# Performance work log

Hardware: AMD Instinct MI355X
Metric: run time of the kernel (lower is better)

Reference implementation:

```python
import jax, jax.numpy as jnp
import numpy as np

B, S, H = 2, 1024, 1024
NH, HD = 8, 128
E, TOPK, MI = 8, 2, 1024
SI = 2 * MI  # shared experts intermediate (n_shared_experts=2)
EPS = 1e-6
THETA = 10000.0


def setup_inputs() -> dict:
    key = jax.random.key(0)
    ks = jax.random.split(key, 16)
    w = lambda k, shp: (0.02 * jax.random.normal(k, shp, dtype=jnp.float32))
    # RoPE tables [S, HD]
    inv_freq = 1.0 / (THETA ** (np.arange(0, HD, 2, dtype=np.float32) / HD))
    t = np.arange(S, dtype=np.float32)
    freqs = np.outer(t, inv_freq)
    emb = np.concatenate([freqs, freqs], axis=-1)
    return {
        "hidden_states": jax.random.normal(ks[0], (B, S, H), dtype=jnp.float32),
        "ln1_w": jnp.ones((H,), jnp.float32),
        "ln2_w": jnp.ones((H,), jnp.float32),
        "q_w": w(ks[1], (H, H)),
        "k_w": w(ks[2], (H, H)),
        "v_w": w(ks[3], (H, H)),
        "o_w": w(ks[4], (H, H)),
        "cos": jnp.asarray(np.cos(emb), jnp.float32),
        "sin": jnp.asarray(np.sin(emb), jnp.float32),
        "gate_w": w(ks[5], (E, H)),
        "eg_w": w(ks[6], (E, MI, H)),
        "eu_w": w(ks[7], (E, MI, H)),
        "ed_w": w(ks[8], (E, H, MI)),
        "sg_w": w(ks[9], (SI, H)),
        "su_w": w(ks[10], (SI, H)),
        "sd_w": w(ks[11], (H, SI)),
    }


def _rmsnorm(x, w):
    return x * jax.lax.rsqrt(jnp.mean(x * x, axis=-1, keepdims=True) + EPS) * w


def _rotate_half(x):
    x1, x2 = jnp.split(x, 2, axis=-1)
    return jnp.concatenate([-x2, x1], axis=-1)


def _attention(x, q_w, k_w, v_w, o_w, cos, sin):
    b, s, h = x.shape
    q = (x @ q_w.T).reshape(b, s, NH, HD)
    k = (x @ k_w.T).reshape(b, s, NH, HD)
    v = (x @ v_w.T).reshape(b, s, NH, HD)
    c = cos[None, :s, None, :]
    sn = sin[None, :s, None, :]
    q = q * c + _rotate_half(q) * sn
    k = k * c + _rotate_half(k) * sn
    scores = jnp.einsum("bqhd,bkhd->bhqk", q, k) / jnp.sqrt(jnp.float32(HD))
    causal = jnp.tril(jnp.ones((s, s), dtype=bool))
    scores = jnp.where(causal[None, None], scores, -jnp.inf)
    p = jax.nn.softmax(scores, axis=-1)
    out = jnp.einsum("bhqk,bkhd->bqhd", p, v).reshape(b, s, h)
    return out @ o_w.T


def _mlp(x, gw, uw, dw):
    return (jax.nn.silu(x @ gw.T) * (x @ uw.T)) @ dw.T


def _moe(x, gate_w, eg_w, eu_w, ed_w, sg_w, su_w, sd_w):
    b, s, h = x.shape
    xt = x.reshape(-1, h)                              # [T, H]
    T = xt.shape[0]
    probs = jax.nn.softmax(xt @ gate_w.T, axis=-1)     # [T, E]
    rw, idx = jax.lax.top_k(probs, TOPK)               # [T, K]
    rw = rw / (jnp.sum(rw, axis=-1, keepdims=True) + 1e-20)  # norm_topk_prob
    # dense combine weights [T, E] (zero for unselected experts)
    w_full = jnp.zeros((T, E), xt.dtype).at[jnp.arange(T)[:, None], idx].add(rw)
    # dense all-expert compute, masked-combined (faithful to per-token loop math)
    g = jax.nn.silu(jnp.einsum("th,eih->tei", xt, eg_w))
    u = jnp.einsum("th,eih->tei", xt, eu_w)
    y = jnp.einsum("tei,ehi->teh", g * u, ed_w)        # [T, E, H]
    routed = jnp.einsum("teh,te->th", y, w_full)
    shared = _mlp(xt, sg_w, su_w, sd_w)
    return (routed + shared).reshape(b, s, h)


def reference(hidden_states, ln1_w, ln2_w, q_w, k_w, v_w, o_w, cos, sin,
              gate_w, eg_w, eu_w, ed_w, sg_w, su_w, sd_w):
    x = hidden_states
    x = x + _attention(_rmsnorm(x, ln1_w), q_w, k_w, v_w, o_w, cos, sin)
    x = x + _moe(_rmsnorm(x, ln2_w), gate_w, eg_w, eu_w, ed_w, sg_w, su_w, sd_w)
    return x
```

## Files before the change

### kernel.cpp

```cpp
#include <hip/hip_runtime.h>

#define B_   2
#define S_   1024
#define H_   1024
#define NH_  8
#define HD_  128
#define E_   8
#define MI_  1024
#define SI_  2048
#define T_   2048
#define CAP_ 2048

typedef unsigned short u16;
typedef __attribute__((ext_vector_type(4))) float f32x4;
typedef __attribute__((ext_vector_type(4))) unsigned short u16x4;
typedef __attribute__((ext_vector_type(8))) unsigned short u16x8;
typedef __attribute__((ext_vector_type(8))) __bf16 bf16x8;

__device__ __forceinline__ u16 f2bf(float f) {
  unsigned int u = __builtin_bit_cast(unsigned int, f);
  u = (u + 0x7fffu + ((u >> 16) & 1u)) >> 16;
  return (u16)u;
}
__device__ __forceinline__ float bf2f(u16 u) {
  return __builtin_bit_cast(float, (unsigned int)u << 16);
}
__device__ __forceinline__ float wave_sum(float v) {
#pragma unroll
  for (int o = 32; o; o >>= 1) v += __shfl_down(v, o, 64);
  return v;
}
__device__ __forceinline__ void gll16(const u16* g, u16* l) {
  __builtin_amdgcn_global_load_lds((const __attribute__((address_space(1))) void*)g,
                                   (__attribute__((address_space(3))) void*)l, 16, 0, 0);
}

__device__ __forceinline__ void cvt_moe_rows(
    int row0, int tid,
    const float* __restrict__ eg_w, const float* __restrict__ eu_w,
    const float* __restrict__ ed_w, const float* __restrict__ sg_w,
    const float* __restrict__ su_w, const float* __restrict__ sd_w,
    u16* __restrict__ egu, u16* __restrict__ edb,
    u16* __restrict__ sgu, u16* __restrict__ sdb) {
  const float* src[8];
  u16* dst[8];
#pragma unroll
  for (int g = 0; g < 8; g++) {
    int row = row0 + g;
    if (row < 20480) {
      int rel = row - 4096;
      int zu = rel >= 8192;
      int r = rel & 8191;
      int e = r >> 10, i = r & 1023;
      int orow = (i >> 4) * 32 + (i & 15) + (zu ? 16 : 0);
      src[g] = (zu ? eu_w : eg_w) + (long)r * 1024;
      dst[g] = egu + ((long)e * 2048 + orow) * 1024;
    } else if (row < 28672) {
      long f = (long)(row - 20480) * 1024;
      src[g] = ed_w + f;
      dst[g] = edb + f;
    } else if (row < 32768) {
      int rel = row - 28672;
      int zu = rel >= 2048;
      int i = rel & 2047;
      int orow = (i >> 4) * 32 + (i & 15) + (zu ? 16 : 0);
      src[g] = (zu ? su_w : sg_w) + (long)i * 1024;
      dst[g] = sgu + (long)orow * 1024;
    } else {
      long f = (long)(row - 32768) * 1024;
      src[g] = sd_w + f;
      dst[g] = sdb + f;
    }
  }
  f32x4 v[8];
#pragma unroll
  for (int g = 0; g < 8; g++)
    v[g] = __builtin_nontemporal_load((const f32x4*)src[g] + tid);
#pragma unroll
  for (int g = 0; g < 8; g++) {
    u16x4 o;
#pragma unroll
    for (int c = 0; c < 4; c++) o[c] = f2bf(v[g][c]);
    ((u16x4*)dst[g])[tid] = o;
  }
}

__global__ void cvt_all(const float* __restrict__ q_w, const float* __restrict__ k_w,
                        const float* __restrict__ v_w, const float* __restrict__ o_w,
                        u16* __restrict__ qwb,
                        const float* __restrict__ hidden, const float* __restrict__ ln1w,
                        u16* __restrict__ xn) {
  int bid = blockIdx.x, tid = threadIdx.x;
  if (bid >= 512) {
    int t = bid - 512;
    f32x4 v = ((const f32x4*)(hidden + (long)t * H_))[tid];
    float ss = v[0]*v[0] + v[1]*v[1] + v[2]*v[2] + v[3]*v[3];
    __shared__ float red[4];
    float s = wave_sum(ss);
    if ((tid & 63) == 0) red[tid >> 6] = s;
    __syncthreads();
    float r = rsqrtf((red[0] + red[1] + red[2] + red[3]) * (1.0f / H_) + 1e-6f);
    f32x4 wv = ((const f32x4*)ln1w)[tid];
    u16x4 o;
#pragma unroll
    for (int c = 0; c < 4; c++) o[c] = f2bf(v[c] * r * wv[c]);
    ((u16x4*)(xn + (long)t * H_))[tid] = o;
    return;
  }
  const float* src[8];
  u16* dst[8];
#pragma unroll
  for (int g = 0; g < 8; g++) {
    int row = bid * 8 + g;
    int seg = row >> 10;
    const float* in = (seg == 0) ? q_w : (seg == 1) ? k_w : (seg == 2) ? v_w : o_w;
    src[g] = in + (long)(row & 1023) * 1024;
    dst[g] = qwb + (long)row * 1024;
  }
  f32x4 v[8];
#pragma unroll
  for (int g = 0; g < 8; g++)
    v[g] = __builtin_nontemporal_load((const f32x4*)src[g] + tid);
#pragma unroll
  for (int g = 0; g < 8; g++) {
    u16x4 o;
#pragma unroll
    for (int c = 0; c < 4; c++) o[c] = f2bf(v[g][c]);
    ((u16x4*)dst[g])[tid] = o;
  }
}

__global__ void rmsnorm2_gate(const float* __restrict__ x1, const float* __restrict__ ln2w,
                              const float* __restrict__ gw, u16* __restrict__ xn,
                              int* __restrict__ eidx, float* __restrict__ aw) {
  int t = blockIdx.x, tid = threadIdx.x;
  int lane = tid & 63, wave = tid >> 6;
  f32x4 v = ((const f32x4*)(x1 + (long)t * H_))[tid];
  float ss = v[0]*v[0] + v[1]*v[1] + v[2]*v[2] + v[3]*v[3];
  __shared__ float redS[4];
  __shared__ float redE[4][E_];
  float s = wave_sum(ss);
  if (lane == 0) redS[wave] = s;
  __syncthreads();
  float r = rsqrtf((redS[0] + redS[1] + redS[2] + redS[3]) * (1.0f / H_) + 1e-6f);
  f32x4 wv = ((const f32x4*)ln2w)[tid];
  float xv[4];
  u16x4 o;
#pragma unroll
  for (int c = 0; c < 4; c++) { xv[c] = v[c] * r * wv[c]; o[c] = f2bf(xv[c]); }
  ((u16x4*)(xn + (long)t * H_))[tid] = o;
  float acc[E_];
#pragma unroll
  for (int e = 0; e < E_; e++) {
    f32x4 g = ((const f32x4*)(gw + (long)e * H_))[tid];
    acc[e] = xv[0]*g[0] + xv[1]*g[1] + xv[2]*g[2] + xv[3]*g[3];
  }
#pragma unroll
  for (int e = 0; e < E_; e++) acc[e] = wave_sum(acc[e]);
  if (lane == 0)
#pragma unroll
    for (int e = 0; e < E_; e++) redE[wave][e] = acc[e];
  __syncthreads();
  if (tid == 0) {
    float l[E_];
#pragma unroll
    for (int e = 0; e < E_; e++) l[e] = redE[0][e] + redE[1][e] + redE[2][e] + redE[3][e];
    float mx = l[0];
#pragma unroll
    for (int e = 1; e < E_; e++) mx = fmaxf(mx, l[e]);
    float p[E_], z = 0.f;
#pragma unroll
    for (int e = 0; e < E_; e++) { p[e] = __expf(l[e] - mx); z += p[e]; }
    int e0 = 0;
#pragma unroll
    for (int e = 1; e < E_; e++) if (p[e] > p[e0]) e0 = e;
    int e1 = (e0 == 0) ? 1 : 0;
#pragma unroll
    for (int e = 0; e < E_; e++) if (e != e0 && p[e] > p[e1]) e1 = e;
    float q0 = p[e0] / z, q1 = p[e1] / z;
    float invs = 1.0f / (q0 + q1 + 1e-20f);
    eidx[t * 2] = e0;
    eidx[t * 2 + 1] = e1;
    aw[t * 2] = q0 * invs;
    aw[t * 2 + 1] = q1 * invs;
  }
}

__global__ __launch_bounds__(256) void route_scan(const int* __restrict__ eidx,
                                                  int* __restrict__ arow,
                                                  int* __restrict__ cursor,
                                                  int* __restrict__ itok,
                                                  int* __restrict__ wlist,
                                                  int* __restrict__ wl256) {
  __shared__ int sc[E_][256];
  int tid = threadIdx.x;
  unsigned c0 = 0, c1 = 0;
  int ebuf[16];
#pragma unroll
  for (int i = 0; i < 16; i++) {
    int e = eidx[tid * 16 + i];
    ebuf[i] = e;
    if (e < 4) c0 += 1u << (8 * e); else c1 += 1u << (8 * (e - 4));
  }
#pragma unroll
  for (int e = 0; e < E_; e++)
    sc[e][tid] = (e < 4) ? (int)((c0 >> (8 * e)) & 0xff) : (int)((c1 >> (8 * (e - 4))) & 0xff);
  __syncthreads();
  for (int st = 1; st < 256; st <<= 1) {
    int v[E_];
#pragma unroll
    for (int e = 0; e < E_; e++) v[e] = (tid >= st) ? sc[e][tid - st] : 0;
    __syncthreads();
#pragma unroll
    for (int e = 0; e < E_; e++) sc[e][tid] += v[e];
    __syncthreads();
  }
  if (tid == 255) {
    int w = 0, w2 = 0;
#pragma unroll
    for (int e = 0; e < E_; e++) {
      int cnt = sc[e][255];
      cursor[e] = cnt;
      int cc = min(cnt, CAP_);
      int nt = (cc + 127) >> 7;
      for (int mt = 0; mt < nt; mt++) wlist[w++] = (e << 8) | mt;
      int nt2 = (cc + 255) >> 8;
      for (int mt = 0; mt < nt2; mt++) wl256[w2++] = (e << 8) | mt;
    }
    for (int mt = 0; mt < 16; mt++) wlist[w++] = (1 << 16) | mt;
    for (; w < 56; w++) wlist[w] = -1;
    for (int mt = 0; mt < 8; mt++) wl256[w2++] = (1 << 16) | mt;
    for (; w2 < 32; w2++) wl256[w2] = -1;
  }
  int base[E_];
#pragma unroll
  for (int e = 0; e < E_; e++) {
    int own = (e < 4) ? (int)((c0 >> (8 * e)) & 0xff) : (int)((c1 >> (8 * (e - 4))) & 0xff);
    base[e] = sc[e][tid] - own;
  }
  __syncthreads();
#pragma unroll
  for (int e = 0; e < E_; e++) sc[e][tid] = base[e];
  __syncthreads();
  unsigned r0 = 0, r1 = 0;
#pragma unroll
  for (int i = 0; i < 16; i++) {
    int e = ebuf[i];
    int run = (e < 4) ? (int)((r0 >> (8 * e)) & 0xff) : (int)((r1 >> (8 * (e - 4))) & 0xff);
    int row = e * CAP_ + sc[e][tid] + run;
    arow[tid * 16 + i] = row;
    itok[row] = (tid * 16 + i) >> 1;
    if (e < 4) r0 += 1u << (8 * e); else r1 += 1u << (8 * (e - 4));
  }
}

__global__ void rope_vtrans(const u16* __restrict__ qkvb, const float* __restrict__ cs,
                            const float* __restrict__ sn, u16* __restrict__ qb,
                            u16* __restrict__ kb, u16* __restrict__ vt) {
  int bid = blockIdx.x, tid = threadIdx.x;
  if (bid < 1024) {
    int z = bid >> 9;
    const u16* src = qkvb + (long)z * 2097152;
    u16* dstb = z ? kb : qb;
    int rb = (bid & 511) * 32 + (tid >> 3);
    int u = tid & 7;
    int h = rb & 7, bs = rb >> 3, s = bs & 1023, b = bs >> 10;
    const u16* row = src + (long)rb * 128;
    int d0 = u * 8;
    u16x8 v1 = *(const u16x8*)(row + d0);
    u16x8 v2 = *(const u16x8*)(row + d0 + 64);
    const float* c1 = cs + s * 128 + d0;
    const float* s1 = sn + s * 128 + d0;
    u16x8 o1, o2;
#pragma unroll
    for (int c = 0; c < 8; c++) {
      float a = bf2f(v1[c]), q2 = bf2f(v2[c]);
      o1[c] = f2bf(a * c1[c] - q2 * s1[c]);
      o2[c] = f2bf(q2 * c1[c + 64] + a * s1[c + 64]);
    }
    u16* orow = dstb + ((long)((b * NH_ + h) * S_ + s)) * HD_;
    *(u16x8*)(orow + d0) = o1;
    *(u16x8*)(orow + d0 + 64) = o2;
  } else {
    int vb = bid - 1024;
    int bh = vb >> 5;
    int rem = vb & 31;
    int s0 = (rem >> 1) * 64, d0 = (rem & 1) * 64;
    int b = bh >> 3, h = bh & 7;
    __shared__ u16 tile[64][68];
    const u16* vsrc = qkvb + 2 * 2097152;
#pragma unroll
    for (int it = 0; it < 4; it++) {
      int idx = it * 256 + tid;
      int r = idx >> 4, c = (idx & 15) * 4;
      u16x4 vv = *(const u16x4*)(vsrc + (((long)(b * S_ + s0 + r)) * NH_ + h) * HD_ + d0 + c);
      *(u16x4*)&tile[r][c] = vv;
    }
    __syncthreads();
#pragma unroll
    for (int it = 0; it < 4; it++) {
      int idx = it * 256 + tid;
      int dr = idx >> 4, sc = (idx & 15) * 4;
      u16x4 ov;
#pragma unroll
      for (int k = 0; k < 4; k++) ov[k] = tile[sc + k][dr];
      *(u16x4*)(vt + ((long)bh * HD_ + d0 + dr) * S_ + s0 + sc) = ov;
    }
  }
}

__global__ __launch_bounds__(256) void flash_cvt(
    const u16* __restrict__ qb, const u16* __restrict__ kb,
    const u16* __restrict__ vt, u16* __restrict__ Po,
    float* __restrict__ Pm, float* __restrict__ Pl,
    const float* __restrict__ eg_w, const float* __restrict__ eu_w,
    const float* __restrict__ ed_w, const float* __restrict__ sg_w,
    const float* __restrict__ su_w, const float* __restrict__ sd_w,
    u16* __restrict__ egu, u16* __restrict__ edb,
    u16* __restrict__ sgu, u16* __restrict__ sdb) {
  int bid = blockIdx.x;
  int tid = threadIdx.x;
  if (bid >= 640) {
    int row0 = 4096 + (bid - 640) * 8;
    cvt_moe_rows(row0, tid, eg_w, eu_w, ed_w, sg_w, su_w, sd_w, egu, edb, sgu, sdb);
    return;
  }
  int item = bid % 40;
  int bh = bid / 40;
  int qt, ch;
  if (item < 4)       { qt = item;                    ch = 0; }
  else if (item < 12) { qt = 4 + ((item - 4) >> 1);   ch = (item - 4) & 1; }
  else if (item < 24) { qt = 8 + (item - 12) / 3;     ch = (item - 12) % 3; }
  else                { qt = 12 + ((item - 24) >> 2); ch = (item - 24) & 3; }
  int j0 = ch * 4, j1 = min(j0 + 4, qt + 1);

  int wavei = tid >> 6, lane = tid & 63;
  int la = lane & 15, qd = lane >> 4;

  __shared__ __align__(16) u16 Ks[64 * 128];
  __shared__ __align__(16) u16 Vs[128 * 64];
  __shared__ __align__(16) u16 Ps[4][16 * 64];

  bf16x8 qf[4];
  const u16* qrow = qb + ((long)bh * S_ + qt * 64 + wavei * 16 + la) * HD_;
#pragma unroll
  for (int ks = 0; ks < 4; ks++)
    qf[ks] = *(const bf16x8*)(qrow + ks * 32 + qd * 8);

  f32x4 oacc[8];
#pragma unroll
  for (int nf = 0; nf < 8; nf++) oacc[nf] = (f32x4){0.f, 0.f, 0.f, 0.f};
  float m_i[4], l_i[4];
#pragma unroll
  for (int r = 0; r < 4; r++) { m_i[r] = -1e30f; l_i[r] = 0.f; }

  const u16* Kbase = kb + (long)bh * S_ * HD_;
  const u16* Vbase = vt + (long)bh * HD_ * S_;
  const float scale = 0.08838834764831845f;
  u16* pw = (u16*)Ps[wavei];
  int swz = la & 7;

  for (int j = j0; j < j1; j++) {
    __syncthreads();
#pragma unroll
    for (int t = 0; t < 4; t++) {
      int blk = t * 4 + wavei;
      int kr = blk * 4 + (lane >> 4);
      int kc = (lane & 15) ^ (kr & 7);
      gll16(Kbase + ((long)j * 64 + kr) * 128 + kc * 8, Ks + blk * 512);
      int vr = blk * 8 + (lane >> 3);
      int vc = (lane & 7) ^ (vr & 7);
      gll16(Vbase + (long)vr * 1024 + j * 64 + vc * 8, Vs + blk * 512);
    }
    __syncthreads();

    f32x4 sacc[4];
#pragma unroll
    for (int jf = 0; jf < 4; jf++) sacc[jf] = (f32x4){0.f, 0.f, 0.f, 0.f};
#pragma unroll
    for (int ks = 0; ks < 4; ks++)
#pragma unroll
      for (int jf = 0; jf < 4; jf++) {
        bf16x8 kfrag = *(const bf16x8*)(Ks + (jf * 16 + la) * 128 + ((ks * 4 + qd) ^ swz) * 8);
        sacc[jf] = __builtin_amdgcn_mfma_f32_16x16x32_bf16(qf[ks], kfrag, sacc[jf], 0, 0, 0);
      }

    float sv[4][4];
    int qglob = qt * 64 + wavei * 16 + qd * 4;
#pragma unroll
    for (int jf = 0; jf < 4; jf++) {
      int kglob = j * 64 + jf * 16 + la;
#pragma unroll
      for (int r = 0; r < 4; r++)
        sv[jf][r] = (kglob <= qglob + r) ? sacc[jf][r] * scale : -1e30f;
    }
    float mnew[4], alpha[4];
#pragma unroll
    for (int r = 0; r < 4; r++) {
      float mx = fmaxf(fmaxf(sv[0][r], sv[1][r]), fmaxf(sv[2][r], sv[3][r]));
#pragma unroll
      for (int o = 1; o < 16; o <<= 1) mx = fmaxf(mx, __shfl_xor(mx, o, 64));
      mnew[r] = fmaxf(m_i[r], mx);
      alpha[r] = __expf(m_i[r] - mnew[r]);
      m_i[r] = mnew[r];
    }
#pragma unroll
    for (int r = 0; r < 4; r++) {
      float sum = 0.f;
#pragma unroll
      for (int jf = 0; jf < 4; jf++) {
        float p = __expf(sv[jf][r] - mnew[r]);
        sv[jf][r] = p;
        sum += p;
      }
#pragma unroll
      for (int o = 1; o < 16; o <<= 1) sum += __shfl_xor(sum, o, 64);
      l_i[r] = l_i[r] * alpha[r] + sum;
    }
#pragma unroll
    for (int jf = 0; jf < 4; jf++)
#pragma unroll
      for (int r = 0; r < 4; r++) {
        int rp = qd * 4 + r;
        int e = jf * 16 + la;
        pw[rp * 64 + (((e >> 3) ^ (rp & 7)) << 3) + (e & 7)] = f2bf(sv[jf][r]);
      }
#pragma unroll
    for (int nf = 0; nf < 8; nf++)
#pragma unroll
      for (int r = 0; r < 4; r++) oacc[nf][r] *= alpha[r];
#pragma unroll
    for (int ks = 0; ks < 2; ks++) {
      bf16x8 pfrag = *(const bf16x8*)(pw + la * 64 + ((ks * 4 + qd) ^ swz) * 8);
#pragma unroll
      for (int nf = 0; nf < 8; nf++) {
        bf16x8 vfrag = *(const bf16x8*)(Vs + (nf * 16 + la) * 64 + (((ks * 4 + qd) & 7) ^ swz) * 8);
        oacc[nf] = __builtin_amdgcn_mfma_f32_16x16x32_bf16(pfrag, vfrag, oacc[nf], 0, 0, 0);
      }
    }
  }

  int pidx = (bh * 16 + qt) * 4 + ch;
  int rowb = wavei * 16 + qd * 4;
  u16* pob = Po + ((long)pidx * 64 + rowb) * 128;
#pragma unroll
  for (int r = 0; r < 4; r++)
#pragma unroll
    for (int nf = 0; nf < 8; nf++)
      pob[(long)r * 128 + nf * 16 + la] = f2bf(oacc[nf][r]);
  if (la == 0)
#pragma unroll
    for (int r = 0; r < 4; r++) {
      Pm[pidx * 64 + rowb + r] = m_i[r];
      Pl[pidx * 64 + rowb + r] = l_i[r];
    }
}

__global__ __launch_bounds__(256) void attn_merge(
    const u16* __restrict__ Po, const float* __restrict__ Pm,
    const float* __restrict__ Pl, u16* __restrict__ attn) {
  int qt = blockIdx.x, bh = blockIdx.y;
  int b = bh >> 3, h = bh & 7;
  int nch = (qt >> 2) + 1;
  int t = threadIdx.x;
  int row = t >> 2, cg = (t & 3) * 32;
  long base = (long)(bh * 16 + qt) * 4;
  float mv[4], wv[4];
  float M = -1e30f;
  for (int c = 0; c < nch; c++) { mv[c] = Pm[(base + c) * 64 + row]; M = fmaxf(M, mv[c]); }
  float L = 0.f;
  for (int c = 0; c < nch; c++) { wv[c] = __expf(mv[c] - M); L += wv[c] * Pl[(base + c) * 64 + row]; }
  float inv = 1.0f / L;
  f32x4 o[8];
#pragma unroll
  for (int k = 0; k < 8; k++) o[k] = (f32x4){0.f, 0.f, 0.f, 0.f};
  for (int c = 0; c < nch; c++) {
    const u16x4* src = (const u16x4*)(Po + ((base + c) * 64 + row) * 128 + cg);
#pragma unroll
    for (int k = 0; k < 8; k++) {
      u16x4 sv = src[k];
#pragma unroll
      for (int e = 0; e < 4; e++) o[k][e] += bf2f(sv[e]) * wv[c];
    }
  }
  u16* dst = attn + ((long)b * S_ + qt * 64 + row) * H_ + h * HD_ + cg;
#pragma unroll
  for (int k = 0; k < 8; k++) {
    u16x4 ov;
#pragma unroll
    for (int c = 0; c < 4; c++) ov[c] = f2bf(o[k][c] * inv);
    ((u16x4*)dst)[k] = ov;
  }
}

__global__ void final_combine(const float* __restrict__ x1, const float* __restrict__ ys,
                              const u16* __restrict__ y, const int* __restrict__ arow,
                              const float* __restrict__ aw, float* __restrict__ out) {
  int t = blockIdx.x;
  int i = threadIdx.x * 4;
  int r0 = arow[t * 2], r1 = arow[t * 2 + 1];
  float w0 = aw[t * 2], w1 = aw[t * 2 + 1];
  f32x4 a = *(const f32x4*)(x1 + (long)t * H_ + i);
  f32x4 b = *(const f32x4*)(ys + (long)t * H_ + i);
  u16x4 y0 = *(const u16x4*)(y + (long)r0 * H_ + i);
  u16x4 y1 = *(const u16x4*)(y + (long)r1 * H_ + i);
  f32x4 o;
#pragma unroll
  for (int c = 0; c < 4; c++)
    o[c] = a[c] + b[c] + w0 * bf2f(y0[c]) + w1 * bf2f(y1[c]);
  *(f32x4*)(out + (long)t * H_ + i) = o;
}

__global__ __launch_bounds__(512) void gemm256(
    const u16* __restrict__ Ag, const u16* __restrict__ Bg, u16* __restrict__ Cg,
    int K, int lda, int ldb, int ldc, long sBz, long sCz,
    const int* __restrict__ itok, const int* __restrict__ wl256,
    const u16* __restrict__ Bg2, u16* __restrict__ Cg2,
    int ldb2, int ldc2, int nx0, int nx1) {
  int wv = wl256[blockIdx.y];
  if (wv < 0) return;
  int kind = wv >> 16;
  if ((int)blockIdx.x >= (kind ? nx1 : nx0)) return;
  int m0 = (wv & 255) << 8;
  int z = (wv >> 8) & 255;
  const u16 *A = Ag, *B;
  u16* C;
  long cbase;
  bool ind;
  if (kind) { B = Bg2; C = Cg2; ldb = ldb2; ldc = ldc2; cbase = 0; ind = false; }
  else      { B = Bg + (long)z * sBz; C = Cg; cbase = (long)z * sCz; ind = true; }
  int n0 = blockIdx.x * 256;

  __shared__ __align__(16) u16 As[2][256 * 64];
  __shared__ __align__(16) u16 Bs[2][256 * 64];
  int tid = threadIdx.x;
  int lane = tid & 63, wave = tid >> 6;
  int wr = wave >> 2, wc = wave & 3;
  int wm = wr * 128, wn = wc * 64;
  int la = lane & 15, qd = lane >> 4;
  int sr = lane >> 3;
  int scs = (lane & 7) ^ (sr & 7);

  const u16* ap[4];
  const u16* bp[4];
#pragma unroll
  for (int r = 0; r < 4; r++) {
    int rloc = m0 + r * 64 + wave * 8 + sr;
    long arow_g = ind ? (long)itok[(long)z * CAP_ + rloc] : (long)rloc;
    ap[r] = A + arow_g * lda + scs * 8;
    bp[r] = B + (long)(n0 + r * 64 + wave * 8 + sr) * ldb + scs * 8;
  }

  f32x4 acc[8][4];
#pragma unroll
  for (int i = 0; i < 8; i++)
#pragma unroll
    for (int j = 0; j < 4; j++) acc[i][j] = (f32x4){0.f, 0.f, 0.f, 0.f};

  auto stage = [&](int buf, int k0) {
#pragma unroll
    for (int r = 0; r < 4; r++)
      gll16(ap[r] + k0, &As[buf][(r * 64 + wave * 8) * 64]);
#pragma unroll
    for (int r = 0; r < 4; r++)
      gll16(bp[r] + k0, &Bs[buf][(r * 64 + wave * 8) * 64]);
  };

  int sw = la & 7;
  int nt = K >> 6;
  int cur = 0;
  stage(0, 0);
  for (int t = 0; t < nt; ++t) {
    if (t + 1 < nt) {
      stage(cur ^ 1, (t + 1) * 64);
      asm volatile("s_waitcnt vmcnt(8)" ::: "memory");
    } else {
      asm volatile("s_waitcnt vmcnt(0)" ::: "memory");
    }
    __builtin_amdgcn_s_barrier();
#pragma unroll
    for (int kk = 0; kk < 2; kk++) {
      bf16x8 af[8], bfv[4];
#pragma unroll
      for (int i = 0; i < 8; i++)
        af[i] = *(const bf16x8*)(&As[cur][0] + (wm + i * 16 + la) * 64 + (((kk * 4 + qd) ^ sw) << 3));
#pragma unroll
      for (int j = 0; j < 4; j++)
        bfv[j] = *(const bf16x8*)(&Bs[cur][0] + (wn + j * 16 + la) * 64 + (((kk * 4 + qd) ^ sw) << 3));
#pragma unroll
      for (int i = 0; i < 8; i++)
#pragma unroll
        for (int j = 0; j < 4; j++)
          acc[i][j] = __builtin_amdgcn_mfma_f32_16x16x32_bf16(af[i], bfv[j], acc[i][j], 0, 0, 0);
    }
    __builtin_amdgcn_s_barrier();
    cur ^= 1;
  }

#pragma unroll
  for (int i = 0; i < 8; i++) {
#pragma unroll
    for (int jp = 0; jp < 2; jp++) {
      int hcol = ((n0 + wn) >> 1) + (jp << 4) + la;
#pragma unroll
      for (int r = 0; r < 4; r++) {
        int row = m0 + wm + i * 16 + qd * 4 + r;
        float g = acc[i][jp * 2][r], u = acc[i][jp * 2 + 1][r];
        float sg = g / (1.f + __expf(-g));
        C[cbase + (long)row * ldc + hcol] = f2bf(sg * u);
      }
    }
  }
}

template <int MT, int STORE_BF16, int ADD_RES, int FUSE_SILU, int IND, int WL>
__global__ __launch_bounds__(256) void gemm_bt(
    const u16* __restrict__ Ag, const u16* __restrict__ Bg, void* __restrict__ Cg,
    const float* __restrict__ Res, int K, int lda, int ldb, int ldc,
    long sAz, long sBz, long sCz, const int* __restrict__ mlimit,
    const int* __restrict__ itok, const int* __restrict__ wlist,
    const u16* __restrict__ Ag2, const u16* __restrict__ Bg2, void* __restrict__ Cg2,
    int lda2, int ldb2, int ldc2, int K2, int nx0, int nx1) {
  constexpr int MR = MT / 32;
  int z = 0, m0, kind = 0;
  const u16 *A, *B;
  void* C;
  long cbase;
  bool ind = (IND != 0);
  if constexpr (WL == 2) {
    int wv = wlist[blockIdx.y];
    if (wv < 0) return;
    kind = wv >> 16;
    if ((int)blockIdx.x >= (kind ? nx1 : nx0)) return;
    m0 = (wv & 255) * MT;
    if (kind) {
      A = Ag2; B = Bg2; C = Cg2;
      lda = lda2; ldb = ldb2; ldc = ldc2; K = K2;
      ind = false;
      cbase = 0;
    } else {
      z = (wv >> 8) & 255;
      A = Ag + (IND ? 0 : z * sAz);
      B = Bg + z * sBz;
      C = Cg;
      cbase = (long)z * sCz;
    }
  } else {
    z = blockIdx.z;
    m0 = blockIdx.y * MT;
    if (mlimit && m0 >= mlimit[z]) return;
    A = Ag + (IND ? 0 : z * sAz);
    B = Bg + z * sBz;
    C = Cg;
    cbase = (long)z * sCz;
  }
  int n0 = blockIdx.x * 128;

  __shared__ __align__(16) u16 As[2][MT * 64];
  __shared__ __align__(16) u16 Bs[2][128 * 64];
  int tid = threadIdx.x;
  int lane = tid & 63, wave = tid >> 6;
  int wm = (wave & 1) * (MT / 2), wn = (wave >> 1) * 64;
  int la = lane & 15, qd = lane >> 4;
  int sr = lane >> 3;
  int scs = (lane & 7) ^ (sr & 7);

  const u16* ap[MT / 32];
  const u16* bp[4];
#pragma unroll
  for (int t = 0; t < MT / 32; t++) {
    int rloc = m0 + t * 32 + wave * 8 + sr;
    long arow_g = (IND && ind) ? (long)itok[(long)z * CAP_ + rloc] : (long)rloc;
    ap[t] = A + arow_g * lda + scs * 8;
  }
#pragma unroll
  for (int t = 0; t < 4; t++)
    bp[t] = B + (long)(n0 + t * 32 + wave * 8 + sr) * ldb + scs * 8;

  f32x4 acc[MR][4];
#pragma unroll
  for (int i = 0; i < MR; i++)
#pragma unroll
    for (int j = 0; j < 4; j++) acc[i][j] = (f32x4){0.f, 0.f, 0.f, 0.f};

  auto stage = [&](int buf, int k0) {
#pragma unroll
    for (int t = 0; t < MT / 32; t++)
      gll16(ap[t] + k0, &As[buf][(t * 32 + wave * 8) * 64]);
#pragma unroll
    for (int t = 0; t < 4; t++)
      gll16(bp[t] + k0, &Bs[buf][(t * 32 + wave * 8) * 64]);
  };

  int sw = la & 7;
  int nt = K >> 6;
  int cur = 0;
  stage(0, 0);
  for (int t = 0; t < nt; ++t) {
    if (t + 1 < nt) {
      stage(cur ^ 1, (t + 1) * 64);
      if constexpr (MT == 128)
        asm volatile("s_waitcnt vmcnt(8)" ::: "memory");
      else
        asm volatile("s_waitcnt vmcnt(6)" ::: "memory");
    } else {
      asm volatile("s_waitcnt vmcnt(0)" ::: "memory");
    }
    __builtin_amdgcn_s_barrier();
#pragma unroll
    for (int kk = 0; kk < 2; kk++) {
      bf16x8 af[MR], bfv[4];
#pragma unroll
      for (int i = 0; i < MR; i++)
        af[i] = *(const bf16x8*)(&As[cur][0] + (wm + i * 16 + la) * 64 + (((kk * 4 + qd) ^ sw) << 3));
#pragma unroll
      for (int j = 0; j < 4; j++)
        bfv[j] = *(const bf16x8*)(&Bs[cur][0] + (wn + j * 16 + la) * 64 + (((kk * 4 + qd) ^ sw) << 3));
#pragma unroll
      for (int i = 0; i < MR; i++)
#pragma unroll
        for (int j = 0; j < 4; j++)
          acc[i][j] = __builtin_amdgcn_mfma_f32_16x16x32_bf16(af[i], bfv[j], acc[i][j], 0, 0, 0);
    }
    __builtin_amdgcn_s_barrier();
    cur ^= 1;
  }

  if (FUSE_SILU) {
#pragma unroll
    for (int i = 0; i < MR; i++) {
#pragma unroll
      for (int jp = 0; jp < 2; jp++) {
        int hcol = ((n0 + wn) >> 1) + (jp << 4) + la;
#pragma unroll
        for (int r = 0; r < 4; r++) {
          int row = m0 + wm + i * 16 + qd * 4 + r;
          float g = acc[i][jp * 2][r], u = acc[i][jp * 2 + 1][r];
          float sg = g / (1.f + __expf(-g));
          ((u16*)C)[cbase + (long)row * ldc + hcol] = f2bf(sg * u);
        }
      }
    }
  } else {
    bool sbf = (WL == 2) ? (kind == 0) : (STORE_BF16 != 0);
#pragma unroll
    for (int i = 0; i < MR; i++) {
#pragma unroll
      for (int j = 0; j < 4; j++) {
        int col = n0 + wn + j * 16 + la;
#pragma unroll
        for (int r = 0; r < 4; r++) {
          int row = m0 + wm + i * 16 + qd * 4 + r;
          float v = acc[i][j][r];
          long ci = cbase + (long)row * ldc + col;
          if (ADD_RES) v += Res[(long)row * ldc + col];
          if (sbf) ((u16*)C)[ci] = f2bf(v);
          else ((float*)C)[ci] = v;
        }
      }
    }
  }
}

extern "C" void kernel_launch(void* const* d_in, const int* in_sizes, int n_in,
                              void* d_out, int out_size, void* d_ws, size_t ws_size,
                              hipStream_t stream) {
  const float* hidden = (const float*)d_in[0];
  const float* ln1w = (const float*)d_in[1];
  const float* ln2w = (const float*)d_in[2];
  const float* q_w = (const float*)d_in[3];
  const float* k_w = (const float*)d_in[4];
  const float* v_w = (const float*)d_in[5];
  const float* o_w = (const float*)d_in[6];
  const float* cosp = (const float*)d_in[7];
  const float* sinp = (const float*)d_in[8];
  const float* gate_w = (const float*)d_in[9];
  const float* eg_w = (const float*)d_in[10];
  const float* eu_w = (const float*)d_in[11];
  const float* ed_w = (const float*)d_in[12];
  const float* sg_w = (const float*)d_in[13];
  const float* su_w = (const float*)d_in[14];
  const float* sd_w = (const float*)d_in[15];
  float* out = (float*)d_out;

  char* w = (char*)d_ws;
  const size_t MB = 1u << 20;
  u16* qwb = (u16*)(w + 0 * MB);
  u16* egu = (u16*)(w + 8 * MB);
  u16* edb = (u16*)(w + 40 * MB);
  u16* sgu = (u16*)(w + 56 * MB);
  u16* sdb = (u16*)(w + 64 * MB);
  float* x1 = (float*)(w + 68 * MB);
  u16* xn = (u16*)(w + 76 * MB);
  u16* attn = (u16*)(w + 80 * MB);
  int* cursor = (int*)(w + 84 * MB);
  int* arow = (int*)(w + 84 * MB + 1024);
  float* aw = (float*)(w + 84 * MB + 20 * 1024);
  int* eidx = (int*)(w + 84 * MB + 40 * 1024);
  int* itok = (int*)(w + 84 * MB + 60 * 1024);
  int* wlist = (int*)(w + 84 * MB + 128 * 1024);
  int* wl256 = (int*)(w + 84 * MB + 132 * 1024);
  u16* qkvb = (u16*)(w + 85 * MB);
  u16* qb = (u16*)(w + 109 * MB);
  u16* kb = (u16*)(w + 113 * MB);
  u16* vt = (u16*)(w + 117 * MB);
  u16* Po = (u16*)(w + 121 * MB);
  float* Pm = (float*)(w + 155 * MB);
  float* Pl = (float*)(w + 156 * MB);
  u16* hbuf = (u16*)(w + 121 * MB);
  u16* y = (u16*)(w + 157 * MB);
  u16* hs = (u16*)(w + 189 * MB);
  float* ys = (float*)(w + 197 * MB);

  const long M1 = 1048576, M2 = 2097152;

  cvt_all<<<2560, 256, 0, stream>>>(q_w, k_w, v_w, o_w, qwb, hidden, ln1w, xn);

  gemm_bt<128, 1, 0, 0, 0, 0><<<dim3(8, 16, 3), 256, 0, stream>>>(
      xn, qwb, qkvb, nullptr, 1024, 1024, 1024, 1024, 0, M1, M2, nullptr, nullptr,
      nullptr, nullptr, nullptr, nullptr, 0, 0, 0, 0, 0, 0);
  rope_vtrans<<<1536, 256, 0, stream>>>(qkvb, cosp, sinp, qb, kb, vt);
  flash_cvt<<<640 + 3840, 256, 0, stream>>>(qb, kb, vt, Po, Pm, Pl,
                                            eg_w, eu_w, ed_w, sg_w, su_w, sd_w,
                                            egu, edb, sgu, sdb);
  attn_merge<<<dim3(16, 16), 256, 0, stream>>>(Po, Pm, Pl, attn);
  gemm_bt<64, 0, 1, 0, 0, 0><<<dim3(8, 32, 1), 256, 0, stream>>>(
      attn, qwb + 3 * M1, x1, hidden, 1024, 1024, 1024, 1024, 0, 0, 0, nullptr, nullptr,
      nullptr, nullptr, nullptr, nullptr, 0, 0, 0, 0, 0, 0);

  rmsnorm2_gate<<<T_, 256, 0, stream>>>(x1, ln2w, gate_w, xn, eidx, aw);
  hipMemsetAsync(itok, 0, E_ * CAP_ * 4, stream);
  route_scan<<<1, 256, 0, stream>>>(eidx, arow, cursor, itok, wlist, wl256);
  gemm256<<<dim3(16, 32, 1), 512, 0, stream>>>(
      xn, egu, hbuf, 1024, 1024, 1024, MI_,
      (long)2 * MI_ * H_, (long)CAP_ * MI_, itok, wl256,
      sgu, hs, 1024, SI_, 8, 16);
  gemm_bt<128, 1, 0, 0, 0, 2><<<dim3(8, 56, 1), 256, 0, stream>>>(
      hbuf, edb, y, nullptr, 1024, 1024, 1024, 1024,
      (long)CAP_ * MI_, (long)H_ * MI_, (long)CAP_ * H_, nullptr, nullptr, wlist,
      hs, sdb, ys, 2048, 2048, 1024, 2048, 8, 8);

  final_combine<<<T_, 256, 0, stream>>>(x1, ys, y, arow, aw, out);
}
```

Measured before the change: 380.6 us.

## Flatten MoE GEMM grids into interleaved 1D tile work lists

The route scan now builds flat per-tile schedules for the gate/up and down GEMMs. Expert tiles are interleaved so consecutive block IDs map to different experts (index e + 8*slot), and the shared-expert tiles are spread across the same slots. The GEMMs launch 1D grids that decode m0, n0 and expert from each entry, replacing the 2D grids that early-exited many blocks on the x dimension. The goal is fewer idle blocks and a more even spread of experts across CUs and XCDs, at the cost of more list-building work in a single-block kernel.

```diff
diff --git a/kernel.cpp b/kernel.cpp
--- a/kernel.cpp
+++ b/kernel.cpp
@@ -190,8 +190,8 @@
                                                   int* __restrict__ arow,
                                                   int* __restrict__ cursor,
                                                   int* __restrict__ itok,
-                                                  int* __restrict__ wlist,
-                                                  int* __restrict__ wl256) {
+                                                  int* __restrict__ wgu,
+                                                  int* __restrict__ wdn) {
   __shared__ int sc[E_][256];
   int tid = threadIdx.x;
   unsigned c0 = 0, c1 = 0;
@@ -215,22 +215,33 @@
     for (int e = 0; e < E_; e++) sc[e][tid] += v[e];
     __syncthreads();
   }
-  if (tid == 255) {
-    int w = 0, w2 = 0;
-#pragma unroll
-    for (int e = 0; e < E_; e++) {
-      int cnt = sc[e][255];
-      cursor[e] = cnt;
-      int cc = min(cnt, CAP_);
-      int nt = (cc + 127) >> 7;
-      for (int mt = 0; mt < nt; mt++) wlist[w++] = (e << 8) | mt;
-      int nt2 = (cc + 255) >> 8;
-      for (int mt = 0; mt < nt2; mt++) wl256[w2++] = (e << 8) | mt;
-    }
-    for (int mt = 0; mt < 16; mt++) wlist[w++] = (1 << 16) | mt;
-    for (; w < 56; w++) wlist[w] = -1;
-    for (int mt = 0; mt < 8; mt++) wl256[w2++] = (1 << 16) | mt;
-    for (; w2 < 32; w2++) wl256[w2] = -1;
+  for (int i = tid; i < 640; i += 256) wgu[i] = -1;
+  for (int i = tid; i < 1152; i += 256) wdn[i] = -1;
+  __syncthreads();
+  if (tid < 8) cursor[tid] = sc[tid][255];
+  for (int i = tid; i < 512; i += 256) {
+    int e = i >> 6, item = i & 63;
+    int mt = item >> 3, nx = item & 7;
+    int nmt = (min(sc[e][255], CAP_) + 255) >> 8;
+    if (mt < nmt) wgu[e + 8 * (mt * 8 + nx)] = (0 << 12) | (e << 8) | (mt << 4) | nx;
+  }
+  if (tid < 128) {
+    int k = tid >> 4, idx = tid & 15;
+    int mi = idx >> 2, ni = idx & 3;
+    int nmt = (min(sc[k][255], CAP_) + 255) >> 8;
+    wgu[k + 8 * (8 * nmt + idx)] = (1 << 12) | ((4 * (k >> 2) + mi) << 4) | (4 * (k & 3) + ni);
+  }
+  for (int i = tid; i < 1024; i += 256) {
+    int e = i >> 7, item = i & 127;
+    int mt = item >> 3, nx = item & 7;
+    int nmt = (min(sc[e][255], CAP_) + 127) >> 7;
+    if (mt < nmt) wdn[e + 8 * (mt * 8 + nx)] = (0 << 16) | (e << 12) | (mt << 5) | nx;
+  }
+  if (tid < 128) {
+    int k = tid >> 4, idx = tid & 15;
+    int mi = idx >> 2, ni = idx & 3;
+    int nmt = (min(sc[k][255], CAP_) + 127) >> 7;
+    wdn[k + 8 * (8 * nmt + idx)] = (1 << 16) | ((4 * (k >> 1) + mi) << 5) | (4 * (k & 1) + ni);
   }
   int base[E_];
 #pragma unroll
@@ -514,22 +525,22 @@
 __global__ __launch_bounds__(512) void gemm256(
     const u16* __restrict__ Ag, const u16* __restrict__ Bg, u16* __restrict__ Cg,
     int K, int lda, int ldb, int ldc, long sBz, long sCz,
-    const int* __restrict__ itok, const int* __restrict__ wl256,
+    const int* __restrict__ itok, const int* __restrict__ wgu,
     const u16* __restrict__ Bg2, u16* __restrict__ Cg2,
-    int ldb2, int ldc2, int nx0, int nx1) {
-  int wv = wl256[blockIdx.y];
-  if (wv < 0) return;
-  int kind = wv >> 16;
-  if ((int)blockIdx.x >= (kind ? nx1 : nx0)) return;
-  int m0 = (wv & 255) << 8;
-  int z = (wv >> 8) & 255;
-  const u16 *A = Ag, *B;
+    int ldb2, int ldc2) {
+  int s = wgu[blockIdx.x];
+  if (s < 0) return;
+  int kind = s >> 12;
+  int z = (s >> 8) & 7;
+  int m0 = ((s >> 4) & 15) << 8;
+  int n0 = (s & 15) << 8;
+  const u16* A = Ag;
+  const u16* B;
   u16* C;
   long cbase;
   bool ind;
   if (kind) { B = Bg2; C = Cg2; ldb = ldb2; ldc = ldc2; cbase = 0; ind = false; }
   else      { B = Bg + (long)z * sBz; C = Cg; cbase = (long)z * sCz; ind = true; }
-  int n0 = blockIdx.x * 256;
 
   __shared__ __align__(16) u16 As[2][256 * 64];
   __shared__ __align__(16) u16 Bs[2][256 * 64];
@@ -620,26 +631,26 @@
     long sAz, long sBz, long sCz, const int* __restrict__ mlimit,
     const int* __restrict__ itok, const int* __restrict__ wlist,
     const u16* __restrict__ Ag2, const u16* __restrict__ Bg2, void* __restrict__ Cg2,
-    int lda2, int ldb2, int ldc2, int K2, int nx0, int nx1) {
+    int lda2, int ldb2, int ldc2, int K2) {
   constexpr int MR = MT / 32;
-  int z = 0, m0, kind = 0;
+  int z = 0, m0, n0, kind = 0;
   const u16 *A, *B;
   void* C;
   long cbase;
   bool ind = (IND != 0);
-  if constexpr (WL == 2) {
-    int wv = wlist[blockIdx.y];
-    if (wv < 0) return;
-    kind = wv >> 16;
-    if ((int)blockIdx.x >= (kind ? nx1 : nx0)) return;
-    m0 = (wv & 255) * MT;
+  if constexpr (WL == 3) {
+    int s = wlist[blockIdx.x];
+    if (s < 0) return;
+    kind = s >> 16;
+    m0 = ((s >> 5) & 127) * MT;
+    n0 = (s & 31) * 128;
     if (kind) {
       A = Ag2; B = Bg2; C = Cg2;
       lda = lda2; ldb = ldb2; ldc = ldc2; K = K2;
       ind = false;
       cbase = 0;
     } else {
-      z = (wv >> 8) & 255;
+      z = (s >> 12) & 7;
       A = Ag + (IND ? 0 : z * sAz);
       B = Bg + z * sBz;
       C = Cg;
@@ -648,13 +659,13 @@
   } else {
     z = blockIdx.z;
     m0 = blockIdx.y * MT;
+    n0 = blockIdx.x * 128;
     if (mlimit && m0 >= mlimit[z]) return;
     A = Ag + (IND ? 0 : z * sAz);
     B = Bg + z * sBz;
     C = Cg;
     cbase = (long)z * sCz;
   }
-  int n0 = blockIdx.x * 128;
 
   __shared__ __align__(16) u16 As[2][MT * 64];
   __shared__ __align__(16) u16 Bs[2][128 * 64];
@@ -742,7 +753,7 @@
       }
     }
   } else {
-    bool sbf = (WL == 2) ? (kind == 0) : (STORE_BF16 != 0);
+    bool sbf = (WL >= 2) ? (kind == 0) : (STORE_BF16 != 0);
 #pragma unroll
     for (int i = 0; i < MR; i++) {
 #pragma unroll
@@ -798,8 +809,8 @@
   float* aw = (float*)(w + 84 * MB + 20 * 1024);
   int* eidx = (int*)(w + 84 * MB + 40 * 1024);
   int* itok = (int*)(w + 84 * MB + 60 * 1024);
-  int* wlist = (int*)(w + 84 * MB + 128 * 1024);
-  int* wl256 = (int*)(w + 84 * MB + 132 * 1024);
+  int* wgu = (int*)(w + 84 * MB + 132 * 1024);
+  int* wdn = (int*)(w + 84 * MB + 136 * 1024);
   u16* qkvb = (u16*)(w + 85 * MB);
   u16* qb = (u16*)(w + 109 * MB);
   u16* kb = (u16*)(w + 113 * MB);
@@ -818,7 +829,7 @@
 
   gemm_bt<128, 1, 0, 0, 0, 0><<<dim3(8, 16, 3), 256, 0, stream>>>(
       xn, qwb, qkvb, nullptr, 1024, 1024, 1024, 1024, 0, M1, M2, nullptr, nullptr,
-      nullptr, nullptr, nullptr, nullptr, 0, 0, 0, 0, 0, 0);
+      nullptr, nullptr, nullptr, nullptr, 0, 0, 0, 0);
   rope_vtrans<<<1536, 256, 0, stream>>>(qkvb, cosp, sinp, qb, kb, vt);
   flash_cvt<<<640 + 3840, 256, 0, stream>>>(qb, kb, vt, Po, Pm, Pl,
                                             eg_w, eu_w, ed_w, sg_w, su_w, sd_w,
@@ -826,19 +837,19 @@
   attn_merge<<<dim3(16, 16), 256, 0, stream>>>(Po, Pm, Pl, attn);
   gemm_bt<64, 0, 1, 0, 0, 0><<<dim3(8, 32, 1), 256, 0, stream>>>(
       attn, qwb + 3 * M1, x1, hidden, 1024, 1024, 1024, 1024, 0, 0, 0, nullptr, nullptr,
-      nullptr, nullptr, nullptr, nullptr, 0, 0, 0, 0, 0, 0);
+      nullptr, nullptr, nullptr, nullptr, 0, 0, 0, 0);
 
   rmsnorm2_gate<<<T_, 256, 0, stream>>>(x1, ln2w, gate_w, xn, eidx, aw);
   hipMemsetAsync(itok, 0, E_ * CAP_ * 4, stream);
-  route_scan<<<1, 256, 0, stream>>>(eidx, arow, cursor, itok, wlist, wl256);
-  gemm256<<<dim3(16, 32, 1), 512, 0, stream>>>(
+  route_scan<<<1, 256, 0, stream>>>(eidx, arow, cursor, itok, wgu, wdn);
+  gemm256<<<640, 512, 0, stream>>>(
       xn, egu, hbuf, 1024, 1024, 1024, MI_,
-      (long)2 * MI_ * H_, (long)CAP_ * MI_, itok, wl256,
-      sgu, hs, 1024, SI_, 8, 16);
-  gemm_bt<128, 1, 0, 0, 0, 2><<<dim3(8, 56, 1), 256, 0, stream>>>(
+      (long)2 * MI_ * H_, (long)CAP_ * MI_, itok, wgu,
+      sgu, hs, 1024, SI_);
+  gemm_bt<128, 1, 0, 0, 0, 3><<<1152, 256, 0, stream>>>(
       hbuf, edb, y, nullptr, 1024, 1024, 1024, 1024,
-      (long)CAP_ * MI_, (long)H_ * MI_, (long)CAP_ * H_, nullptr, nullptr, wlist,
-      hs, sdb, ys, 2048, 2048, 1024, 2048, 8, 8);
+      (long)CAP_ * MI_, (long)H_ * MI_, (long)CAP_ * H_, nullptr, nullptr, wdn,
+      hs, sdb, ys, 2048, 2048, 1024, 2048);
 
   final_combine<<<T_, 256, 0, stream>>>(x1, ys, y, arow, aw, out);
 }
```

Measured after the change: 376.7 us. No clear change (-1.0%).
